# Kernel optimization log

Hardware: AMD Instinct MI355X
Metric: run time of the kernel (lower is better)

Reference implementation:

```python
import jax, jax.numpy as jnp
import numpy as np
import math

B, L, D, H = 2, 2048, 1024, 16
HS = D // H  # head size 64


def setup_inputs() -> dict:
    key = jax.random.key(0)
    ks = jax.random.split(key, 4)
    s = 1.0 / math.sqrt(D)
    return {
        "x": jax.random.normal(ks[0], (B, L, D), dtype=jnp.float32),
        "mask": jnp.zeros((B, 1, L, L), dtype=jnp.float32),
        "Wq": jax.random.normal(ks[1], (D, D), dtype=jnp.float32) * s,
        "bq": jnp.zeros((D,), dtype=jnp.float32),
        "Wk": jax.random.normal(ks[2], (D, D), dtype=jnp.float32) * s,
        "bk": jnp.zeros((D,), dtype=jnp.float32),
        "Wv": jax.random.normal(ks[3], (D, D), dtype=jnp.float32) * s,
        "bv": jnp.zeros((D,), dtype=jnp.float32),
    }


def reference(x, mask, Wq, bq, Wk, bk, Wv, bv):
    # projections: torch Linear is x @ W.T + b
    q = (x @ Wq.T + bq).reshape(B, L, H, HS).transpose(0, 2, 1, 3)  # [B,H,L,hs]
    k = (x @ Wk.T + bk).reshape(B, L, H, HS).transpose(0, 2, 1, 3)
    v = (x @ Wv.T + bv).reshape(B, L, H, HS).transpose(0, 2, 1, 3)
    scores = jnp.einsum("bhqd,bhkd->bhqk", q, k) / math.sqrt(HS) + mask
    attn = jax.nn.softmax(scores, axis=-1)  # dropout p=0.0 -> identity
    out = jnp.einsum("bhqk,bhkd->bhqd", attn, v)
    return out.transpose(0, 2, 1, 3).reshape(B, L, D)
```

## Files before the change

kernel.cpp:

```cpp
#include <hip/hip_runtime.h>
#include <cstdint>

#define SEQ 2048
#define DMODEL 1024
#define NHEAD 16
#define HEADSZ 64

typedef __attribute__((ext_vector_type(4))) float f32x4;
typedef __attribute__((ext_vector_type(16))) float f32x16;
typedef __attribute__((ext_vector_type(8))) short short8;
typedef __attribute__((ext_vector_type(4))) unsigned short u16x4;
typedef __attribute__((ext_vector_type(4))) unsigned int u32x4;

#define AS1 __attribute__((address_space(1)))
#define AS3 __attribute__((address_space(3)))

__device__ __forceinline__ void gload_lds16(const void* g, void* l) {
  __builtin_amdgcn_global_load_lds((const AS1 void*)g, (AS3 void*)l, 16, 0, 0);
}

__device__ __forceinline__ unsigned short f2bf(float f) {
  unsigned u = __float_as_uint(f);
  u += 0x7fffu + ((u >> 16) & 1u);
  return (unsigned short)(u >> 16);
}

__device__ __forceinline__ unsigned pack2bf(float lo, float hi) {
  return (unsigned)f2bf(lo) | ((unsigned)f2bf(hi) << 16);
}

__global__ __launch_bounds__(256) void convert_kernel(
    const float* __restrict__ x, const float* __restrict__ wq,
    const float* __restrict__ wk, const float* __restrict__ wv,
    unsigned short* __restrict__ xb, unsigned short* __restrict__ wb) {
  const long i = ((long)blockIdx.x * 256 + threadIdx.x) * 4;
  const float* src;
  unsigned short* dst;
  if (i < (1L << 22)) {
    src = x + i; dst = xb + i;
  } else {
    const long j = i - (1L << 22);
    dst = wb + j;
    if (j < (1L << 20))        src = wq + j;
    else if (j < (2L << 20))   src = wk + (j - (1L << 20));
    else                       src = wv + (j - (2L << 20));
  }
  f32x4 v = *(const f32x4*)src;
  u16x4 o;
  o.x = f2bf(v.x); o.y = f2bf(v.y); o.z = f2bf(v.z); o.w = f2bf(v.w);
  *(u16x4*)dst = o;
}

__global__ __launch_bounds__(256) void qkv_gemm(
    const unsigned short* __restrict__ xb, const unsigned short* __restrict__ wb,
    const float* __restrict__ bq, const float* __restrict__ bk,
    const float* __restrict__ bv,
    unsigned short* __restrict__ qo, unsigned short* __restrict__ ko,
    unsigned short* __restrict__ vto) {
  __shared__ __attribute__((aligned(16))) unsigned short Sh[2][128 * 64];
  unsigned short* As = &Sh[0][0];
  unsigned short* Bs = &Sh[1][0];

  const int bid = blockIdx.x;
  const int swz = (bid & 7) * 96 + (bid >> 3);
  const int tm = swz / 24, tn = swz % 24;
  const int m0 = tm * 128, n0 = tn * 128;
  const int tsel = n0 >> 10;
  const int t = threadIdx.x;
  const int lane = t & 63, wid = t >> 6;
  const int wr = wid >> 1, wc = wid & 1;
  const int r16 = lane & 15, g4 = lane >> 4;

  f32x4 acc[4][4] = {};

  const unsigned short* ga0 = xb + (long)(m0 + (t >> 3)) * 1024 + (t & 7) * 8;
  const unsigned short* gb0 = wb + (long)(n0 + (t >> 3)) * 1024 + (t & 7) * 8;
  char* lA = (char*)As + wid * 1024;
  char* lB = (char*)Bs + wid * 1024;

  for (int ks = 0; ks < 16; ++ks) {
    const unsigned short* ga = ga0 + ks * 64;
    const unsigned short* gb = gb0 + ks * 64;
#pragma unroll
    for (int r = 0; r < 4; ++r) {
      gload_lds16(ga + r * 32 * 1024, lA + r * 4096);
      gload_lds16(gb + r * 32 * 1024, lB + r * 4096);
    }
    __syncthreads();
#pragma unroll
    for (int kk = 0; kk < 2; ++kk) {
      short8 af[4], bf[4];
#pragma unroll
      for (int mi = 0; mi < 4; ++mi)
        af[mi] = *(const short8*)((const char*)As +
                 (wr * 64 + mi * 16 + r16) * 128 + kk * 64 + g4 * 16);
#pragma unroll
      for (int ni = 0; ni < 4; ++ni)
        bf[ni] = *(const short8*)((const char*)Bs +
                 (wc * 64 + ni * 16 + r16) * 128 + kk * 64 + g4 * 16);
      if (tsel < 2) {
#pragma unroll
        for (int mi = 0; mi < 4; ++mi)
#pragma unroll
          for (int ni = 0; ni < 4; ++ni)
            acc[mi][ni] = __builtin_amdgcn_mfma_f32_16x16x32_bf16(
                bf[ni], af[mi], acc[mi][ni], 0, 0, 0);
      } else {
#pragma unroll
        for (int mi = 0; mi < 4; ++mi)
#pragma unroll
          for (int ni = 0; ni < 4; ++ni)
            acc[mi][ni] = __builtin_amdgcn_mfma_f32_16x16x32_bf16(
                af[mi], bf[ni], acc[mi][ni], 0, 0, 0);
      }
    }
    __syncthreads();
  }

  const int bb = m0 >> 11;
  const int lbase = m0 & 2047;
  const int h0n = n0 & 1023;
  unsigned short* T = As;

  if (tsel < 2) {
    const float* bias = tsel == 0 ? bq : bk;
    unsigned short* dst01 = tsel == 0 ? qo : ko;
#pragma unroll
    for (int ni = 0; ni < 4; ++ni) {
      const int nlb = wc * 64 + ni * 16 + g4 * 4;
      const f32x4 b4 = *(const f32x4*)(bias + h0n + nlb);
#pragma unroll
      for (int mi = 0; mi < 4; ++mi) {
        const int ml = wr * 64 + mi * 16 + r16;
        u16x4 pk;
#pragma unroll
        for (int i = 0; i < 4; ++i) pk[i] = f2bf(acc[mi][ni][i] + b4[i]);
        int byteoff = ml * 256 + nlb * 2;
        byteoff ^= (ml & 7) << 4;
        *(u16x4*)((char*)T + byteoff) = pk;
      }
    }
    __syncthreads();
#pragma unroll
    for (int p = 0; p < 8; ++p) {
      const int ml = p * 16 + (t >> 4);
      int byteoff = ml * 256 + ((t & 15) << 4);
      byteoff ^= (ml & 7) << 4;
      short8 row = *(const short8*)((const char*)T + byteoff);
      const int nd = h0n + (t & 15) * 8;
      const int h = nd >> 6, hs = nd & 63;
      *(short8*)(dst01 + ((long)(bb * NHEAD + h) * SEQ + lbase + ml) * 64 + hs) = row;
    }
  } else {
#pragma unroll
    for (int ni = 0; ni < 4; ++ni) {
      const int nl = wc * 64 + ni * 16 + r16;
      const float bval = bv[h0n + nl];
#pragma unroll
      for (int mi = 0; mi < 4; ++mi) {
        const int mlb = wr * 64 + mi * 16 + g4 * 4;
        u16x4 pk;
#pragma unroll
        for (int i = 0; i < 4; ++i) pk[i] = f2bf(acc[mi][ni][i] + bval);
        int byteoff = nl * 256 + mlb * 2;
        byteoff ^= (nl & 7) << 4;
        *(u16x4*)((char*)T + byteoff) = pk;
      }
    }
    __syncthreads();
#pragma unroll
    for (int p = 0; p < 8; ++p) {
      const int nl = p * 16 + (t >> 4);
      int byteoff = nl * 256 + ((t & 15) << 4);
      byteoff ^= (nl & 7) << 4;
      short8 row = *(const short8*)((const char*)T + byteoff);
      const int nd = h0n + nl;
      const int h = nd >> 6, hs = nd & 63;
      *(short8*)(vto + ((((long)(bb * NHEAD + h)) << 6) + hs) * SEQ + lbase +
                 (t & 15) * 8) = row;
    }
  }
}

__global__ __launch_bounds__(256, 2) void attn_kernel(
    const unsigned short* __restrict__ qb, const unsigned short* __restrict__ kb,
    const unsigned short* __restrict__ vtb, const float* __restrict__ mask,
    float* __restrict__ out) {
  __shared__ __attribute__((aligned(16))) char lds[34816];
  unsigned short* Ks = (unsigned short*)lds;
  unsigned short* Vs = (unsigned short*)(lds + 16384);

  const int bid = blockIdx.x;
  const int swz = (bid & 7) * 64 + (bid >> 3);
  const int h = swz & 15, grp = swz >> 4;
  const int qt = grp & 15, b = grp >> 4;
  const int bh = b * NHEAD + h;

  const int t = threadIdx.x;
  const int lane = t & 63, w = t >> 6;
  const int lq = lane & 31;
  const int hi = lane >> 5;

  const unsigned short* qg = qb + (long)bh * SEQ * 64;
  const unsigned short* kg = kb + (long)bh * SEQ * 64;
  const unsigned short* vg = vtb + (long)bh * 64 * SEQ;
  const int q0 = qt * 128 + w * 32;
  const float* mrow = mask + (long)b * SEQ * SEQ + (long)(q0 + lq) * SEQ;

  auto stageKV = [&](int kt, int buf) {
#pragma unroll
    for (int r = 0; r < 2; ++r) {
      const int row = w * 16 + r * 8 + (lane >> 3);
      const int gsw = ((lane & 7) ^ (row & 7)) * 8;
      gload_lds16(kg + (long)(kt * 64 + row) * 64 + gsw,
                  (char*)Ks + buf * 8192 + w * 2048 + r * 1024);
      gload_lds16(vg + (long)row * SEQ + kt * 64 + gsw,
                  (char*)Vs + buf * 8192 + w * 2048 + r * 1024);
    }
  };

  stageKV(0, 0);

  short8 qf[4];
#pragma unroll
  for (int kk = 0; kk < 4; ++kk)
    qf[kk] = *(const short8*)(qg + (long)(q0 + lq) * 64 + hi * 8 + kk * 16);

  f32x16 oa0 = {}, oa1 = {};
  float m_st = -1e30f, l_st = 0.f;
  const float L2E = 1.4426950408889634f;

  __syncthreads();

  int cur = 0;
  for (int kt = 0; kt < 32; ++kt) {
    if (kt < 31) stageKV(kt + 1, cur ^ 1);

    const char* Kb = (const char*)Ks + cur * 8192;
    const char* Vb = (const char*)Vs + cur * 8192;

    f32x4 mv[2][4];
#pragma unroll
    for (int k2 = 0; k2 < 2; ++k2)
#pragma unroll
      for (int g = 0; g < 4; ++g)
        mv[k2][g] = *(const f32x4*)(mrow + kt * 64 + k2 * 32 + g * 8 + hi * 4);

    f32x16 sa0 = {}, sa1 = {};
    __builtin_amdgcn_s_setprio(1);
#pragma unroll
    for (int kk = 0; kk < 4; ++kk) {
      const int r0 = lq;
      short8 kf0 = *(const short8*)(Kb + r0 * 128 + (((hi + 2 * kk) ^ (r0 & 7)) << 4));
      sa0 = __builtin_amdgcn_mfma_f32_32x32x16_bf16(kf0, qf[kk], sa0, 0, 0, 0);
      const int r1 = 32 + lq;
      short8 kf1 = *(const short8*)(Kb + r1 * 128 + (((hi + 2 * kk) ^ (r1 & 7)) << 4));
      sa1 = __builtin_amdgcn_mfma_f32_32x32x16_bf16(kf1, qf[kk], sa1, 0, 0, 0);
    }
    __builtin_amdgcn_s_setprio(0);

    float s[32];
#pragma unroll
    for (int r = 0; r < 16; ++r)
      s[r] = sa0[r] * 0.125f + mv[0][r >> 2][r & 3];
#pragma unroll
    for (int r = 0; r < 16; ++r)
      s[16 + r] = sa1[r] * 0.125f + mv[1][r >> 2][r & 3];

    float pm0 = s[0], pm1 = s[1], pm2 = s[2], pm3 = s[3];
#pragma unroll
    for (int r = 4; r < 32; r += 4) {
      pm0 = fmaxf(pm0, s[r]);     pm1 = fmaxf(pm1, s[r + 1]);
      pm2 = fmaxf(pm2, s[r + 2]); pm3 = fmaxf(pm3, s[r + 3]);
    }
    float pm = fmaxf(fmaxf(pm0, pm1), fmaxf(pm2, pm3));
    pm = fmaxf(pm, __shfl_xor(pm, 32, 64));

    if (!__all(pm <= m_st + 8.0f)) {
      const float mn = fmaxf(m_st, pm);
      const float alpha = exp2f((m_st - mn) * L2E);
      m_st = mn;
      l_st *= alpha;
#pragma unroll
      for (int r = 0; r < 16; ++r) { oa0[r] *= alpha; oa1[r] *= alpha; }
    }

    const float nml2e = -m_st * L2E;
    float rs0 = 0.f, rs1 = 0.f, rs2 = 0.f, rs3 = 0.f;
#pragma unroll
    for (int r = 0; r < 32; r += 4) {
      const float p0 = exp2f(fmaf(s[r], L2E, nml2e));
      const float p1 = exp2f(fmaf(s[r + 1], L2E, nml2e));
      const float p2 = exp2f(fmaf(s[r + 2], L2E, nml2e));
      const float p3 = exp2f(fmaf(s[r + 3], L2E, nml2e));
      s[r] = p0; s[r + 1] = p1; s[r + 2] = p2; s[r + 3] = p3;
      rs0 += p0; rs1 += p1; rs2 += p2; rs3 += p3;
    }
    float rs = (rs0 + rs1) + (rs2 + rs3);
    rs += __shfl_xor(rs, 32, 64);
    l_st += rs;

    u32x4 pw[4];
#pragma unroll
    for (int kk = 0; kk < 4; ++kk) {
      const int base = kk * 8;
      const unsigned X  = pack2bf(s[base + 0], s[base + 1]);
      const unsigned X2 = pack2bf(s[base + 2], s[base + 3]);
      const unsigned Y  = pack2bf(s[base + 4], s[base + 5]);
      const unsigned Y2 = pack2bf(s[base + 6], s[base + 7]);
      const unsigned Xp  = __shfl_xor(X, 32, 64);
      const unsigned X2p = __shfl_xor(X2, 32, 64);
      const unsigned Yp  = __shfl_xor(Y, 32, 64);
      const unsigned Y2p = __shfl_xor(Y2, 32, 64);
      pw[kk][0] = hi ? Yp : X;
      pw[kk][1] = hi ? Y2p : X2;
      pw[kk][2] = hi ? Y : Xp;
      pw[kk][3] = hi ? Y2 : X2p;
    }

    __builtin_amdgcn_s_setprio(1);
#pragma unroll
    for (int kk = 0; kk < 4; ++kk) {
      const short8 pf = __builtin_bit_cast(short8, pw[kk]);
      const int r0 = lq;
      short8 vf0 = *(const short8*)(Vb + r0 * 128 + (((hi + 2 * kk) ^ (r0 & 7)) << 4));
      oa0 = __builtin_amdgcn_mfma_f32_32x32x16_bf16(vf0, pf, oa0, 0, 0, 0);
      const int r1 = 32 + lq;
      short8 vf1 = *(const short8*)(Vb + r1 * 128 + (((hi + 2 * kk) ^ (r1 & 7)) << 4));
      oa1 = __builtin_amdgcn_mfma_f32_32x32x16_bf16(vf1, pf, oa1, 0, 0, 0);
    }
    __builtin_amdgcn_s_setprio(0);

    __syncthreads();
    cur ^= 1;
  }

  __syncthreads();
  float* ot = (float*)lds + w * (32 * 68);
  const float inv_l = 1.f / l_st;
#pragma unroll
  for (int g = 0; g < 4; ++g) {
    f32x4 v0, v1;
#pragma unroll
    for (int j = 0; j < 4; ++j) { v0[j] = oa0[g * 4 + j] * inv_l;
                                  v1[j] = oa1[g * 4 + j] * inv_l; }
    *(f32x4*)(ot + lq * 68 + g * 8 + hi * 4) = v0;
    *(f32x4*)(ot + lq * 68 + 32 + g * 8 + hi * 4) = v1;
  }
  asm volatile("s_waitcnt lgkmcnt(0)" ::: "memory");
  float* ob = out + (long)b * SEQ * DMODEL + (long)q0 * DMODEL + h * 64;
#pragma unroll
  for (int j = 0; j < 8; ++j) {
    const int qr = j * 4 + (lane >> 4);
    f32x4 v4 = *(const f32x4*)(ot + qr * 68 + (lane & 15) * 4);
    *(f32x4*)(ob + (long)qr * DMODEL + (lane & 15) * 4) = v4;
  }
}

extern "C" void kernel_launch(void* const* d_in, const int* in_sizes, int n_in,
                              void* d_out, int out_size, void* d_ws, size_t ws_size,
                              hipStream_t stream) {
  const float* x    = (const float*)d_in[0];
  const float* mask = (const float*)d_in[1];
  const float* Wq   = (const float*)d_in[2];
  const float* bq   = (const float*)d_in[3];
  const float* Wk   = (const float*)d_in[4];
  const float* bk   = (const float*)d_in[5];
  const float* Wv   = (const float*)d_in[6];
  const float* bv   = (const float*)d_in[7];
  float* out = (float*)d_out;

  char* ws = (char*)d_ws;
  unsigned short* xb  = (unsigned short*)(ws);
  unsigned short* wb  = (unsigned short*)(ws + (8L << 20));
  unsigned short* qo  = (unsigned short*)(ws + (14L << 20));
  unsigned short* ko  = (unsigned short*)(ws + (22L << 20));
  unsigned short* vto = (unsigned short*)(ws + (30L << 20));

  convert_kernel<<<7168, 256, 0, stream>>>(x, Wq, Wk, Wv, xb, wb);
  qkv_gemm<<<768, 256, 0, stream>>>(xb, wb, bq, bk, bv, qo, ko, vto);
  attn_kernel<<<512, 256, 0, stream>>>(qo, ko, vto, mask, out);
}
```

Measured before the change: 246.9 us.

## Double-buffer QKV GEMM LDS tiles and XOR-swizzle columns to avoid bank conflicts

The QKV projection GEMM now keeps two LDS stages and issues the global-to-LDS loads for the next k-slice before computing on the current one, so memory latency overlaps the MFMA work. The global source column is XOR-permuted by row, and fragment reads apply the same XOR, which spreads LDS reads across banks. LDS use doubles to 64KB, which may reduce occupancy. The loop keeps only one barrier per iteration, so correctness depends on that barrier covering both the async loads and the buffer reuse.

Result: faster. 237.9 us (-3.6%).

```diff
diff --git a/kernel.cpp b/kernel.cpp
--- a/kernel.cpp
+++ b/kernel.cpp
@@ -57,9 +57,7 @@
     const float* __restrict__ bv,
     unsigned short* __restrict__ qo, unsigned short* __restrict__ ko,
     unsigned short* __restrict__ vto) {
-  __shared__ __attribute__((aligned(16))) unsigned short Sh[2][128 * 64];
-  unsigned short* As = &Sh[0][0];
-  unsigned short* Bs = &Sh[1][0];
+  __shared__ __attribute__((aligned(16))) unsigned short Sh[2][2][128 * 64];
 
   const int bid = blockIdx.x;
   const int swz = (bid & 7) * 96 + (bid >> 3);
@@ -70,34 +68,45 @@
   const int lane = t & 63, wid = t >> 6;
   const int wr = wid >> 1, wc = wid & 1;
   const int r16 = lane & 15, g4 = lane >> 4;
+  const int swzr = r16 & 7;
 
   f32x4 acc[4][4] = {};
 
-  const unsigned short* ga0 = xb + (long)(m0 + (t >> 3)) * 1024 + (t & 7) * 8;
-  const unsigned short* gb0 = wb + (long)(n0 + (t >> 3)) * 1024 + (t & 7) * 8;
-  char* lA = (char*)As + wid * 1024;
-  char* lB = (char*)Bs + wid * 1024;
-
-  for (int ks = 0; ks < 16; ++ks) {
+  const int csel = ((t & 7) ^ ((t >> 3) & 7)) * 8;
+  const unsigned short* ga0 = xb + (long)(m0 + (t >> 3)) * 1024 + csel;
+  const unsigned short* gb0 = wb + (long)(n0 + (t >> 3)) * 1024 + csel;
+
+  auto stage = [&](int ks, int buf) {
     const unsigned short* ga = ga0 + ks * 64;
     const unsigned short* gb = gb0 + ks * 64;
+    char* lA = (char*)&Sh[buf][0][0] + wid * 1024;
+    char* lB = (char*)&Sh[buf][1][0] + wid * 1024;
 #pragma unroll
     for (int r = 0; r < 4; ++r) {
       gload_lds16(ga + r * 32 * 1024, lA + r * 4096);
       gload_lds16(gb + r * 32 * 1024, lB + r * 4096);
     }
-    __syncthreads();
+  };
+
+  stage(0, 0);
+  __syncthreads();
+
+  int cur = 0;
+  for (int ks = 0; ks < 16; ++ks) {
+    if (ks < 15) stage(ks + 1, cur ^ 1);
+    const char* As = (const char*)&Sh[cur][0][0];
+    const char* Bs = (const char*)&Sh[cur][1][0];
 #pragma unroll
     for (int kk = 0; kk < 2; ++kk) {
       short8 af[4], bf[4];
 #pragma unroll
       for (int mi = 0; mi < 4; ++mi)
-        af[mi] = *(const short8*)((const char*)As +
-                 (wr * 64 + mi * 16 + r16) * 128 + kk * 64 + g4 * 16);
+        af[mi] = *(const short8*)(As + (wr * 64 + mi * 16 + r16) * 128 +
+                 (((kk * 4 + g4) ^ swzr) << 4));
 #pragma unroll
       for (int ni = 0; ni < 4; ++ni)
-        bf[ni] = *(const short8*)((const char*)Bs +
-                 (wc * 64 + ni * 16 + r16) * 128 + kk * 64 + g4 * 16);
+        bf[ni] = *(const short8*)(Bs + (wc * 64 + ni * 16 + r16) * 128 +
+                 (((kk * 4 + g4) ^ swzr) << 4));
       if (tsel < 2) {
 #pragma unroll
         for (int mi = 0; mi < 4; ++mi)
@@ -115,12 +124,13 @@
       }
     }
     __syncthreads();
+    cur ^= 1;
   }
 
   const int bb = m0 >> 11;
   const int lbase = m0 & 2047;
   const int h0n = n0 & 1023;
-  unsigned short* T = As;
+  unsigned short* T = &Sh[0][0][0];
 
   if (tsel < 2) {
     const float* bias = tsel == 0 ? bq : bk;
```
